# Kernel optimization log

Hardware: AMD Instinct MI355X
Metric: run time of the kernel (lower is better)

## Reference

```python
import jax, jax.numpy as jnp
import numpy as np

B, C, H, Wd, IN_CAPS = 128, 32, 12, 12, 8
OUT_CH, OUT_CAPS, ROUTING_ITERS = 10, 16, 3


def setup_inputs() -> dict:
    key = jax.random.key(0)
    k1, k2 = jax.random.split(key)
    x = jax.random.normal(k1, (B, C, H, Wd, IN_CAPS), dtype=jnp.float32)
    W = jax.random.normal(k2, (1, 1, C, OUT_CH, OUT_CAPS, IN_CAPS), dtype=jnp.float32)
    return {"x": x, "W": W}


def _squash(s):
    # s: [..., out_caps]
    sn = jnp.sum(s * s, axis=-1, keepdims=True)
    return sn * s / ((1.0 + sn) * jnp.sqrt(sn))


def reference(x, W):
    b = x.shape[0]
    # [B, H, W, C, in_caps]
    u = jnp.transpose(x, (0, 2, 3, 1, 4))
    Wm = W[0, 0]  # [C, out_ch, out_caps, in_caps]
    # u_hat[b,h,w,c,o,p] = sum_q Wm[c,o,p,q] * u[b,h,w,c,q]
    u_hat = jnp.einsum('copq,bhwcq->bhwcop', Wm, u)
    u_hat = u_hat.reshape(b, -1, OUT_CH, OUT_CAPS)  # [B, N, O, P]

    b_ij = jnp.zeros(u_hat.shape[:-1], dtype=u_hat.dtype)  # [B, N, O]
    v_j = None
    for i in range(ROUTING_ITERS):
        c_ij = jax.nn.softmax(b_ij, axis=-1)[..., None]  # [B, N, O, 1]
        s_j = jnp.sum(c_ij * u_hat, axis=1)              # [B, O, P]
        v_j = _squash(s_j)                               # [B, O, P]
        if i < ROUTING_ITERS - 1:
            a_j = jnp.sum(u_hat * v_j[:, None], axis=-1)  # [B, N, O]
            b_ij = b_ij + a_j
    return v_j
```

## Files before the change

kernel.cpp:

```cpp
#include <hip/hip_runtime.h>


#define BB 128
#define CC 32
#define HWN 144
#define HWH 72
#define QQ 8
#define OO 10
#define PP 16
#define OH 5

__device__ float    g_sx[3 * BB * 2 * OO * PP];
__device__ unsigned g_cnt[BB * 32];

__device__ __forceinline__ float squash16(float s) {
    float sn = s * s;
#pragma unroll
    for (int m = 1; m <= 8; m <<= 1) sn += __shfl_xor(sn, m);
    return s * (sqrtf(sn) / (1.f + sn));
}

__global__ __launch_bounds__(512, 1)
void digitcaps_routing(const float* __restrict__ x, const float* __restrict__ Wm,
                       float* __restrict__ out) {
    const int bh  = blockIdx.x;
    const int b   = blockIdx.y;
    const int tid = threadIdx.x;

    __shared__ float usum_s[CC * QQ];
    __shared__ float Wv_s[CC * OO * QQ];
    __shared__ float t_s[CC * OO * QQ];
    __shared__ float v_s[OO * PP];
    __shared__ float ps2_s[2 * OO * PP];

    {
        const int c = tid >> 4, slot = tid & 15;
        const float* xc = x + (((size_t)b * CC + c) * HWN + bh * HWH) * QQ;
        float us[QQ];
#pragma unroll
        for (int q = 0; q < QQ; ++q) us[q] = 0.f;
#pragma unroll
        for (int i = 0; i < 5; ++i) {
            const int hwl = slot + (i << 4);
            if (hwl < HWH) {
                const float4* p4 = (const float4*)(xc + hwl * QQ);
                float4 a = p4[0], d = p4[1];
                us[0] += a.x; us[1] += a.y; us[2] += a.z; us[3] += a.w;
                us[4] += d.x; us[5] += d.y; us[6] += d.z; us[7] += d.w;
            }
        }
#pragma unroll
        for (int m = 1; m <= 8; m <<= 1) {
#pragma unroll
            for (int q = 0; q < QQ; ++q) us[q] += __shfl_xor(us[q], m);
        }
        if (slot == 0) {
#pragma unroll
            for (int q = 0; q < QQ; ++q) usum_s[c * QQ + q] = us[q];
        }
    }
    __syncthreads();

    const int hc    = tid >> 4;
    const int hslot = (tid >> 1) & 7;
    const int oh    = tid & 1;
    const int obase = oh * OH;
    const float* xhc = x + (((size_t)b * CC + hc) * HWN + bh * HWH) * QQ;

    for (int ph = 0; ph < 3; ++ph) {
        if (tid < 2 * OO * PP) {
            const int h   = tid >= OO * PP;
            const int idx = h ? tid - OO * PP : tid;
            const int o = idx >> 4, p = idx & 15;
            const int c0 = h * 16;
            float s = 0.f;
#pragma unroll
            for (int k = 0; k < 16; ++k) {
                const int cc = c0 + k;
                const float4* w4 = (const float4*)(Wm + (((cc * OO + o) * PP + p) * QQ));
                float4 w0 = w4[0], w1 = w4[1];
                const float* src = (ph == 0) ? &usum_s[cc * QQ]
                                             : &t_s[(cc * OO + o) * QQ];
                s += w0.x * src[0] + w0.y * src[1] + w0.z * src[2] + w0.w * src[3]
                   + w1.x * src[4] + w1.y * src[5] + w1.z * src[6] + w1.w * src[7];
            }
            ps2_s[tid] = s;
        }
        __syncthreads();

        const int spin = (ph < 2) ? 1 : (bh == 0);
        float sown = 0.f;
        if (tid < OO * PP) {
            sown = ps2_s[tid] + ps2_s[OO * PP + tid];
            __hip_atomic_store(&g_sx[(((size_t)ph * BB + b) * 2 + bh) * (OO * PP) + tid],
                               sown, __ATOMIC_RELAXED, __HIP_MEMORY_SCOPE_AGENT);
        }
        __syncthreads();
        if (tid == 0) {
            unsigned t = __hip_atomic_fetch_add(&g_cnt[b * 32], 1u,
                             __ATOMIC_RELAXED, __HIP_MEMORY_SCOPE_AGENT);
            if (spin) {
                const unsigned target = (t / 2u + 1u) * 2u;
                while (__hip_atomic_load(&g_cnt[b * 32], __ATOMIC_RELAXED,
                                         __HIP_MEMORY_SCOPE_AGENT) < target)
                    __builtin_amdgcn_s_sleep(1);
            }
        }
        __syncthreads();
        if (!spin) break;

        if (tid < OO * PP) {
            float soth = __hip_atomic_load(
                &g_sx[(((size_t)ph * BB + b) * 2 + (1 - bh)) * (OO * PP) + tid],
                __ATOMIC_RELAXED, __HIP_MEMORY_SCOPE_AGENT);
            float s = sown + soth;
            if (ph == 0) s *= 0.1f;
            const float v = squash16(s);
            if (ph == 2) { out[(size_t)b * (OO * PP) + tid] = v; }
            else         { v_s[tid] = v; }
        }
        if (ph == 2) break;
        __syncthreads();

        if (tid < CC * OO) {
            const int cc = tid / OO, o = tid - cc * OO;
            float acc[QQ];
#pragma unroll
            for (int q = 0; q < QQ; ++q) acc[q] = 0.f;
            const float* wp = Wm + ((cc * OO + o) * PP) * QQ;
#pragma unroll
            for (int p = 0; p < PP; ++p) {
                const float vv = v_s[o * PP + p];
                const float4* w4 = (const float4*)(wp + p * QQ);
                float4 w0 = w4[0], w1 = w4[1];
                acc[0] += vv * w0.x; acc[1] += vv * w0.y; acc[2] += vv * w0.z; acc[3] += vv * w0.w;
                acc[4] += vv * w1.x; acc[5] += vv * w1.y; acc[6] += vv * w1.z; acc[7] += vv * w1.w;
            }
            float* dst = Wv_s + (cc * OO + o) * QQ;
            if (ph == 0) {
#pragma unroll
                for (int q = 0; q < QQ; ++q) dst[q] = acc[q];
            } else {
#pragma unroll
                for (int q = 0; q < QQ; ++q) dst[q] += acc[q];
            }
        }
        __syncthreads();

        float wv[OH][QQ];
#pragma unroll
        for (int j = 0; j < OH; ++j)
#pragma unroll
            for (int q = 0; q < QQ; ++q)
                wv[j][q] = Wv_s[(hc * OO + obase + j) * QQ + q];

        float tl[OH][QQ];
#pragma unroll
        for (int j = 0; j < OH; ++j)
#pragma unroll
            for (int q = 0; q < QQ; ++q) tl[j][q] = 0.f;

#pragma unroll 3
        for (int i = 0; i < 9; ++i) {
            const int hwl = hslot + (i << 3);
            const float4* p4 = (const float4*)(xhc + hwl * QQ);
            float4 a = p4[0], d = p4[1];
            float u[QQ] = {a.x, a.y, a.z, a.w, d.x, d.y, d.z, d.w};
            float lg[OH];
#pragma unroll
            for (int j = 0; j < OH; ++j) {
                float t = 0.f;
#pragma unroll
                for (int q = 0; q < QQ; ++q) t += u[q] * wv[j][q];
                lg[j] = t;
            }
            float pm = fmaxf(fmaxf(fmaxf(lg[0], lg[1]), fmaxf(lg[2], lg[3])), lg[4]);
            pm = fmaxf(pm, __shfl_xor(pm, 1));
            float psum = 0.f;
#pragma unroll
            for (int j = 0; j < OH; ++j) { lg[j] = __expf(lg[j] - pm); psum += lg[j]; }
            psum += __shfl_xor(psum, 1);
            const float inv = 1.f / psum;
#pragma unroll
            for (int j = 0; j < OH; ++j) {
                const float cij = lg[j] * inv;
#pragma unroll
                for (int q = 0; q < QQ; ++q) tl[j][q] += cij * u[q];
            }
        }
#pragma unroll
        for (int m = 2; m <= 8; m <<= 1) {
#pragma unroll
            for (int j = 0; j < OH; ++j)
#pragma unroll
                for (int q = 0; q < QQ; ++q) tl[j][q] += __shfl_xor(tl[j][q], m);
        }
        if (hslot == 0) {
#pragma unroll
            for (int j = 0; j < OH; ++j)
#pragma unroll
                for (int q = 0; q < QQ; ++q)
                    t_s[(hc * OO + obase + j) * QQ + q] = tl[j][q];
        }
        __syncthreads();
    }
}

extern "C" void kernel_launch(void* const* d_in, const int* in_sizes, int n_in,
                              void* d_out, int out_size, void* d_ws, size_t ws_size,
                              hipStream_t stream) {
    const float* x  = (const float*)d_in[0];
    const float* Wm = (const float*)d_in[1];
    float* out      = (float*)d_out;
    digitcaps_routing<<<dim3(2, BB), 512, 0, stream>>>(x, Wm, out);
}
```

Baseline: 99.53 us.

## Split each batch's spatial work across four cooperating blocks instead of two

Measured after the change: 126.4 us. 1.27x slower.

```diff
diff --git a/kernel.cpp b/kernel.cpp
--- a/kernel.cpp
+++ b/kernel.cpp
@@ -4,13 +4,14 @@
 #define BB 128
 #define CC 32
 #define HWN 144
-#define HWH 72
+#define NSP 4
+#define HWQ 36
 #define QQ 8
 #define OO 10
 #define PP 16
 #define OH 5
 
-__device__ float    g_sx[3 * BB * 2 * OO * PP];
+__device__ float    g_sx[3 * BB * NSP * OO * PP];
 __device__ unsigned g_cnt[BB * 32];
 
 __device__ __forceinline__ float squash16(float s) {
@@ -20,10 +21,10 @@
     return s * (sqrtf(sn) / (1.f + sn));
 }
 
-__global__ __launch_bounds__(512, 1)
+__global__ __launch_bounds__(512, 2)
 void digitcaps_routing(const float* __restrict__ x, const float* __restrict__ Wm,
                        float* __restrict__ out) {
-    const int bh  = blockIdx.x;
+    const int bq  = blockIdx.x;
     const int b   = blockIdx.y;
     const int tid = threadIdx.x;
 
@@ -35,14 +36,14 @@
 
     {
         const int c = tid >> 4, slot = tid & 15;
-        const float* xc = x + (((size_t)b * CC + c) * HWN + bh * HWH) * QQ;
+        const float* xc = x + (((size_t)b * CC + c) * HWN + bq * HWQ) * QQ;
         float us[QQ];
 #pragma unroll
         for (int q = 0; q < QQ; ++q) us[q] = 0.f;
 #pragma unroll
-        for (int i = 0; i < 5; ++i) {
+        for (int i = 0; i < 3; ++i) {
             const int hwl = slot + (i << 4);
-            if (hwl < HWH) {
+            if (hwl < HWQ) {
                 const float4* p4 = (const float4*)(xc + hwl * QQ);
                 float4 a = p4[0], d = p4[1];
                 us[0] += a.x; us[1] += a.y; us[2] += a.z; us[3] += a.w;
@@ -65,7 +66,7 @@
     const int hslot = (tid >> 1) & 7;
     const int oh    = tid & 1;
     const int obase = oh * OH;
-    const float* xhc = x + (((size_t)b * CC + hc) * HWN + bh * HWH) * QQ;
+    const float* xhc = x + (((size_t)b * CC + hc) * HWN + bq * HWQ) * QQ;
 
     for (int ph = 0; ph < 3; ++ph) {
         if (tid < 2 * OO * PP) {
@@ -88,11 +89,11 @@
         }
         __syncthreads();
 
-        const int spin = (ph < 2) ? 1 : (bh == 0);
+        const int spin = (ph < 2) ? 1 : (bq == 0);
         float sown = 0.f;
         if (tid < OO * PP) {
             sown = ps2_s[tid] + ps2_s[OO * PP + tid];
-            __hip_atomic_store(&g_sx[(((size_t)ph * BB + b) * 2 + bh) * (OO * PP) + tid],
+            __hip_atomic_store(&g_sx[(((size_t)ph * BB + b) * NSP + bq) * (OO * PP) + tid],
                                sown, __ATOMIC_RELAXED, __HIP_MEMORY_SCOPE_AGENT);
         }
         __syncthreads();
@@ -100,7 +101,7 @@
             unsigned t = __hip_atomic_fetch_add(&g_cnt[b * 32], 1u,
                              __ATOMIC_RELAXED, __HIP_MEMORY_SCOPE_AGENT);
             if (spin) {
-                const unsigned target = (t / 2u + 1u) * 2u;
+                const unsigned target = (t / NSP + 1u) * NSP;
                 while (__hip_atomic_load(&g_cnt[b * 32], __ATOMIC_RELAXED,
                                          __HIP_MEMORY_SCOPE_AGENT) < target)
                     __builtin_amdgcn_s_sleep(1);
@@ -110,10 +111,14 @@
         if (!spin) break;
 
         if (tid < OO * PP) {
-            float soth = __hip_atomic_load(
-                &g_sx[(((size_t)ph * BB + b) * 2 + (1 - bh)) * (OO * PP) + tid],
-                __ATOMIC_RELAXED, __HIP_MEMORY_SCOPE_AGENT);
-            float s = sown + soth;
+            float s = sown;
+#pragma unroll
+            for (int g = 0; g < NSP; ++g) {
+                if (g == bq) continue;
+                s += __hip_atomic_load(
+                    &g_sx[(((size_t)ph * BB + b) * NSP + g) * (OO * PP) + tid],
+                    __ATOMIC_RELAXED, __HIP_MEMORY_SCOPE_AGENT);
+            }
             if (ph == 0) s *= 0.1f;
             const float v = squash16(s);
             if (ph == 2) { out[(size_t)b * (OO * PP) + tid] = v; }
@@ -160,32 +165,34 @@
 #pragma unroll
             for (int q = 0; q < QQ; ++q) tl[j][q] = 0.f;
 
-#pragma unroll 3
-        for (int i = 0; i < 9; ++i) {
+#pragma unroll
+        for (int i = 0; i < 5; ++i) {
             const int hwl = hslot + (i << 3);
-            const float4* p4 = (const float4*)(xhc + hwl * QQ);
-            float4 a = p4[0], d = p4[1];
-            float u[QQ] = {a.x, a.y, a.z, a.w, d.x, d.y, d.z, d.w};
-            float lg[OH];
-#pragma unroll
-            for (int j = 0; j < OH; ++j) {
-                float t = 0.f;
-#pragma unroll
-                for (int q = 0; q < QQ; ++q) t += u[q] * wv[j][q];
-                lg[j] = t;
-            }
-            float pm = fmaxf(fmaxf(fmaxf(lg[0], lg[1]), fmaxf(lg[2], lg[3])), lg[4]);
-            pm = fmaxf(pm, __shfl_xor(pm, 1));
-            float psum = 0.f;
-#pragma unroll
-            for (int j = 0; j < OH; ++j) { lg[j] = __expf(lg[j] - pm); psum += lg[j]; }
-            psum += __shfl_xor(psum, 1);
-            const float inv = 1.f / psum;
-#pragma unroll
-            for (int j = 0; j < OH; ++j) {
-                const float cij = lg[j] * inv;
-#pragma unroll
-                for (int q = 0; q < QQ; ++q) tl[j][q] += cij * u[q];
+            if (hwl < HWQ) {
+                const float4* p4 = (const float4*)(xhc + hwl * QQ);
+                float4 a = p4[0], d = p4[1];
+                float u[QQ] = {a.x, a.y, a.z, a.w, d.x, d.y, d.z, d.w};
+                float lg[OH];
+#pragma unroll
+                for (int j = 0; j < OH; ++j) {
+                    float t = 0.f;
+#pragma unroll
+                    for (int q = 0; q < QQ; ++q) t += u[q] * wv[j][q];
+                    lg[j] = t;
+                }
+                float pm = fmaxf(fmaxf(fmaxf(lg[0], lg[1]), fmaxf(lg[2], lg[3])), lg[4]);
+                pm = fmaxf(pm, __shfl_xor(pm, 1));
+                float psum = 0.f;
+#pragma unroll
+                for (int j = 0; j < OH; ++j) { lg[j] = __expf(lg[j] - pm); psum += lg[j]; }
+                psum += __shfl_xor(psum, 1);
+                const float inv = 1.f / psum;
+#pragma unroll
+                for (int j = 0; j < OH; ++j) {
+                    const float cij = lg[j] * inv;
+#pragma unroll
+                    for (int q = 0; q < QQ; ++q) tl[j][q] += cij * u[q];
+                }
             }
         }
 #pragma unroll
@@ -212,5 +219,5 @@
     const float* x  = (const float*)d_in[0];
     const float* Wm = (const float*)d_in[1];
     float* out      = (float*)d_out;
-    digitcaps_routing<<<dim3(2, BB), 512, 0, stream>>>(x, Wm, out);
+    digitcaps_routing<<<dim3(NSP, BB), 512, 0, stream>>>(x, Wm, out);
 }
```

## Split work across channel halves, stage W slice in LDS, drop softmax max

Applied to the files above, without the earlier changes.

New measurement: 92.29 us. 1.08x faster.

```diff
diff --git a/kernel.cpp b/kernel.cpp
--- a/kernel.cpp
+++ b/kernel.cpp
@@ -3,8 +3,8 @@
 
 #define BB 128
 #define CC 32
+#define CL 16
 #define HWN 144
-#define HWH 72
 #define QQ 8
 #define OO 10
 #define PP 16
@@ -23,34 +23,42 @@
 __global__ __launch_bounds__(512, 1)
 void digitcaps_routing(const float* __restrict__ x, const float* __restrict__ Wm,
                        float* __restrict__ out) {
-    const int bh  = blockIdx.x;
-    const int b   = blockIdx.y;
+    const int b   = blockIdx.x;
+    const int ch  = blockIdx.y;
     const int tid = threadIdx.x;
 
-    __shared__ float usum_s[CC * QQ];
-    __shared__ float Wv_s[CC * OO * QQ];
-    __shared__ float t_s[CC * OO * QQ];
+    __shared__ float Wm_s[CL * OO * PP * QQ];
+    __shared__ float usum_s[CL * QQ];
+    __shared__ float Wv_s[CL * OO * QQ];
+    __shared__ float t_s[CL * OO * QQ];
     __shared__ float v_s[OO * PP];
     __shared__ float ps2_s[2 * OO * PP];
 
     {
-        const int c = tid >> 4, slot = tid & 15;
-        const float* xc = x + (((size_t)b * CC + c) * HWN + bh * HWH) * QQ;
+        const float4* src = (const float4*)(Wm + (size_t)ch * (CL * OO * PP * QQ));
+        float4* dst = (float4*)Wm_s;
+#pragma unroll
+        for (int k = 0; k < 10; ++k) dst[tid + (k << 9)] = src[tid + (k << 9)];
+    }
+
+    {
+        const int c = tid >> 5, slot = tid & 31;
+        const float* xc = x + ((size_t)b * CC + ch * CL + c) * (HWN * QQ);
         float us[QQ];
 #pragma unroll
         for (int q = 0; q < QQ; ++q) us[q] = 0.f;
 #pragma unroll
         for (int i = 0; i < 5; ++i) {
-            const int hwl = slot + (i << 4);
-            if (hwl < HWH) {
-                const float4* p4 = (const float4*)(xc + hwl * QQ);
+            const int hw = slot + (i << 5);
+            if (hw < HWN) {
+                const float4* p4 = (const float4*)(xc + hw * QQ);
                 float4 a = p4[0], d = p4[1];
                 us[0] += a.x; us[1] += a.y; us[2] += a.z; us[3] += a.w;
                 us[4] += d.x; us[5] += d.y; us[6] += d.z; us[7] += d.w;
             }
         }
 #pragma unroll
-        for (int m = 1; m <= 8; m <<= 1) {
+        for (int m = 1; m <= 16; m <<= 1) {
 #pragma unroll
             for (int q = 0; q < QQ; ++q) us[q] += __shfl_xor(us[q], m);
         }
@@ -61,23 +69,23 @@
     }
     __syncthreads();
 
-    const int hc    = tid >> 4;
-    const int hslot = (tid >> 1) & 7;
+    const int hc    = tid >> 5;
+    const int hslot = (tid >> 1) & 15;
     const int oh    = tid & 1;
     const int obase = oh * OH;
-    const float* xhc = x + (((size_t)b * CC + hc) * HWN + bh * HWH) * QQ;
+    const float* xhc = x + ((size_t)b * CC + ch * CL + hc) * (HWN * QQ);
 
     for (int ph = 0; ph < 3; ++ph) {
         if (tid < 2 * OO * PP) {
             const int h   = tid >= OO * PP;
             const int idx = h ? tid - OO * PP : tid;
             const int o = idx >> 4, p = idx & 15;
-            const int c0 = h * 16;
+            const int c0 = h * 8;
             float s = 0.f;
 #pragma unroll
-            for (int k = 0; k < 16; ++k) {
+            for (int k = 0; k < 8; ++k) {
                 const int cc = c0 + k;
-                const float4* w4 = (const float4*)(Wm + (((cc * OO + o) * PP + p) * QQ));
+                const float4* w4 = (const float4*)(Wm_s + (((cc * OO + o) * PP + p) * QQ));
                 float4 w0 = w4[0], w1 = w4[1];
                 const float* src = (ph == 0) ? &usum_s[cc * QQ]
                                              : &t_s[(cc * OO + o) * QQ];
@@ -88,11 +96,11 @@
         }
         __syncthreads();
 
-        const int spin = (ph < 2) ? 1 : (bh == 0);
+        const int spin = (ph < 2) ? 1 : (ch == 0);
         float sown = 0.f;
         if (tid < OO * PP) {
             sown = ps2_s[tid] + ps2_s[OO * PP + tid];
-            __hip_atomic_store(&g_sx[(((size_t)ph * BB + b) * 2 + bh) * (OO * PP) + tid],
+            __hip_atomic_store(&g_sx[(((size_t)ph * BB + b) * 2 + ch) * (OO * PP) + tid],
                                sown, __ATOMIC_RELAXED, __HIP_MEMORY_SCOPE_AGENT);
         }
         __syncthreads();
@@ -107,11 +115,11 @@
             }
         }
         __syncthreads();
-        if (!spin) break;
+        if (!spin) return;
 
         if (tid < OO * PP) {
             float soth = __hip_atomic_load(
-                &g_sx[(((size_t)ph * BB + b) * 2 + (1 - bh)) * (OO * PP) + tid],
+                &g_sx[(((size_t)ph * BB + b) * 2 + (1 - ch)) * (OO * PP) + tid],
                 __ATOMIC_RELAXED, __HIP_MEMORY_SCOPE_AGENT);
             float s = sown + soth;
             if (ph == 0) s *= 0.1f;
@@ -119,15 +127,15 @@
             if (ph == 2) { out[(size_t)b * (OO * PP) + tid] = v; }
             else         { v_s[tid] = v; }
         }
-        if (ph == 2) break;
-        __syncthreads();
-
-        if (tid < CC * OO) {
-            const int cc = tid / OO, o = tid - cc * OO;
+        if (ph == 2) return;
+        __syncthreads();
+
+        if (tid < CL * OO) {
+            const int cl = tid / OO, o = tid - cl * OO;
             float acc[QQ];
 #pragma unroll
             for (int q = 0; q < QQ; ++q) acc[q] = 0.f;
-            const float* wp = Wm + ((cc * OO + o) * PP) * QQ;
+            const float* wp = Wm_s + ((cl * OO + o) * PP) * QQ;
 #pragma unroll
             for (int p = 0; p < PP; ++p) {
                 const float vv = v_s[o * PP + p];
@@ -136,7 +144,7 @@
                 acc[0] += vv * w0.x; acc[1] += vv * w0.y; acc[2] += vv * w0.z; acc[3] += vv * w0.w;
                 acc[4] += vv * w1.x; acc[5] += vv * w1.y; acc[6] += vv * w1.z; acc[7] += vv * w1.w;
             }
-            float* dst = Wv_s + (cc * OO + o) * QQ;
+            float* dst = Wv_s + (cl * OO + o) * QQ;
             if (ph == 0) {
 #pragma unroll
                 for (int q = 0; q < QQ; ++q) dst[q] = acc[q];
@@ -162,8 +170,8 @@
 
 #pragma unroll 3
         for (int i = 0; i < 9; ++i) {
-            const int hwl = hslot + (i << 3);
-            const float4* p4 = (const float4*)(xhc + hwl * QQ);
+            const int hw = hslot + (i << 4);
+            const float4* p4 = (const float4*)(xhc + hw * QQ);
             float4 a = p4[0], d = p4[1];
             float u[QQ] = {a.x, a.y, a.z, a.w, d.x, d.y, d.z, d.w};
             float lg[OH];
@@ -172,13 +180,9 @@
                 float t = 0.f;
 #pragma unroll
                 for (int q = 0; q < QQ; ++q) t += u[q] * wv[j][q];
-                lg[j] = t;
-            }
-            float pm = fmaxf(fmaxf(fmaxf(lg[0], lg[1]), fmaxf(lg[2], lg[3])), lg[4]);
-            pm = fmaxf(pm, __shfl_xor(pm, 1));
-            float psum = 0.f;
-#pragma unroll
-            for (int j = 0; j < OH; ++j) { lg[j] = __expf(lg[j] - pm); psum += lg[j]; }
+                lg[j] = __expf(t);
+            }
+            float psum = ((lg[0] + lg[1]) + (lg[2] + lg[3])) + lg[4];
             psum += __shfl_xor(psum, 1);
             const float inv = 1.f / psum;
 #pragma unroll
@@ -189,7 +193,7 @@
             }
         }
 #pragma unroll
-        for (int m = 2; m <= 8; m <<= 1) {
+        for (int m = 2; m <= 16; m <<= 1) {
 #pragma unroll
             for (int j = 0; j < OH; ++j)
 #pragma unroll
@@ -212,5 +216,5 @@
     const float* x  = (const float*)d_in[0];
     const float* Wm = (const float*)d_in[1];
     float* out      = (float*)d_out;
-    digitcaps_routing<<<dim3(2, BB), 512, 0, stream>>>(x, Wm, out);
+    digitcaps_routing<<<dim3(BB, 2), 512, 0, stream>>>(x, Wm, out);
 }
```
